# Kernel optimization log

Measured on AMD Instinct MI355X. Metric: run time of the kernel, lower is better.

Reference implementation:

```python
import jax, jax.numpy as jnp
import numpy as np

NEG_BIG = -9e15  # matches torch -9000000000000000.0

def setup_inputs() -> dict:
    key = jax.random.key(0)
    k1, k2, k3, k4 = jax.random.split(key, 4)
    B, N, F_IN, F_OUT = 8, 2048, 128, 64
    x = jax.random.normal(k1, (B, N, F_IN), dtype=jnp.float32)
    adj = jax.random.randint(k2, (B, N, N), 0, 2, dtype=jnp.int32)
    # xavier_uniform-style init for params
    limW = float(np.sqrt(6.0 / (F_IN + F_OUT)))
    W = jax.random.uniform(k3, (F_IN, F_OUT), minval=-limW, maxval=limW, dtype=jnp.float32)
    lima = float(np.sqrt(6.0 / (2 * F_OUT + 1)))
    a = jax.random.uniform(k4, (2 * F_OUT, 1), minval=-lima, maxval=lima, dtype=jnp.float32)
    return {"x": x, "adj": adj, "W": W, "a": a}

def reference(x, adj, W, a):
    # x: [B, N, F_in], adj: [B, N, N], W: [F_in, F_out], a: [2*F_out, 1]
    h = jnp.einsum('bnf,fo->bno', x, W)            # [B, N, F_out]
    F_out = W.shape[1]
    # The repeat/cat construction computes a_input[b,i,j] = [h_i ; h_j], so
    # a_input @ a decomposes into f1_i + f2_j without the O(N^2 * 2F) tensor.
    f1 = h @ a[:F_out, 0]                          # [B, N]
    f2 = h @ a[F_out:, 0]                          # [B, N]
    e = jnp.tanh(f1[:, :, None] + f2[:, None, :])  # [B, N, N]
    att = jnp.where(adj > 0, e, NEG_BIG)
    att = jax.nn.softmax(att, axis=2)              # [B, N, N]
    h_prime = jnp.einsum('bmn,bno->bmo', att, h)   # [B, N, F_out]
    return jax.nn.elu(h_prime)                     # concat=True branch
```

## Files before the change

### kernel.cpp

```cpp
#include <hip/hip_runtime.h>
#include <math.h>

#define BB 8
#define NN 2048
#define FIN 128
#define FOUT 64
#define TI 16
#define TJ 512
#define TJP (TJ + 8)
#define NTILE (NN / TJ)
#define NW (NN / 32)

typedef short bf16x8 __attribute__((ext_vector_type(8)));
typedef float f32x4 __attribute__((ext_vector_type(4)));

__device__ __forceinline__ float exp_tanh(float z) {
    float zc = fminf(fmaxf(z, -15.f), 15.f);
    float u = __expf(zc + zc);
    float tn = (u - 1.f) * __builtin_amdgcn_rcpf(u + 1.f);
    return __expf(tn);
}

__device__ __forceinline__ unsigned short f2bf(float x) {
    union { float f; unsigned u; } v; v.f = x;
    unsigned r = v.u + 0x7FFF + ((v.u >> 16) & 1);
    return (unsigned short)(r >> 16);
}

__global__ __launch_bounds__(256, 2) void gat_k1(const float* __restrict__ x,
                                                 const float* __restrict__ W,
                                                 const float* __restrict__ a,
                                                 unsigned short* __restrict__ ht,
                                                 float* __restrict__ f1,
                                                 float* __restrict__ f2) {
    __shared__ __attribute__((aligned(16))) float Wl[FIN][FOUT];
    __shared__ __attribute__((aligned(16))) float xs[16][FIN];
    int t = threadIdx.x;

    const float4* W4 = (const float4*)W;
    float4* Wl4 = (float4*)&Wl[0][0];
#pragma unroll
    for (int kk = 0; kk < 8; ++kk) Wl4[t + 256 * kk] = W4[t + 256 * kk];

    size_t row0 = (size_t)blockIdx.x * 16;
    const float4* x4 = (const float4*)(x + row0 * FIN);
    float4* xs4 = (float4*)&xs[0][0];
#pragma unroll
    for (int kk = 0; kk < 2; ++kk) xs4[t + 256 * kk] = x4[t + 256 * kk];
    __syncthreads();

    int c = t & 63;
    int rq = t >> 6;
    float acc[4] = {0.f, 0.f, 0.f, 0.f};
#pragma unroll 8
    for (int k = 0; k < FIN; ++k) {
        float wv = Wl[k][c];
        acc[0] = fmaf(xs[rq][k], wv, acc[0]);
        acc[1] = fmaf(xs[rq + 4][k], wv, acc[1]);
        acc[2] = fmaf(xs[rq + 8][k], wv, acc[2]);
        acc[3] = fmaf(xs[rq + 12][k], wv, acc[3]);
    }
    float a1c = a[c], a2c = a[FOUT + c];
#pragma unroll
    for (int m = 0; m < 4; ++m) {
        size_t bn = row0 + rq + 4 * m;
        int b = (int)(bn >> 11);
        int n = (int)(bn & 2047);
        ht[((size_t)b * FOUT + c) * NN + n] = f2bf(acc[m]);
        float p1 = acc[m] * a1c;
        float p2 = acc[m] * a2c;
#pragma unroll
        for (int off = 32; off > 0; off >>= 1) {
            p1 += __shfl_down(p1, off, 64);
            p2 += __shfl_down(p2, off, 64);
        }
        if (c == 0) { f1[bn] = p1; f2[bn] = p2; }
    }
}

__global__ __launch_bounds__(256) void gat_pack(const int* __restrict__ adj,
                                                unsigned int* __restrict__ adjm) {
    __shared__ __attribute__((aligned(4))) unsigned char nib[2048];
    int t = threadIdx.x;
    const int4* a4 = (const int4*)adj + (size_t)blockIdx.x * 2048;
#pragma unroll
    for (int kk = 0; kk < 8; ++kk) {
        int4 v = a4[t + 256 * kk];
        unsigned n = (unsigned)(v.x > 0) | ((unsigned)(v.y > 0) << 1) |
                     ((unsigned)(v.z > 0) << 2) | ((unsigned)(v.w > 0) << 3);
        nib[t + 256 * kk] = (unsigned char)n;
    }
    __syncthreads();
    const unsigned* nu = (const unsigned*)nib;
    unsigned u0 = nu[2 * t], u1 = nu[2 * t + 1];
    unsigned m = (u0 & 0xFu) | (((u0 >> 8) & 0xFu) << 4) |
                 (((u0 >> 16) & 0xFu) << 8) | (((u0 >> 24) & 0xFu) << 12) |
                 ((u1 & 0xFu) << 16) | (((u1 >> 8) & 0xFu) << 20) |
                 (((u1 >> 16) & 0xFu) << 24) | (((u1 >> 24) & 0xFu) << 28);
    adjm[(size_t)blockIdx.x * 256 + t] = m;
}

__global__ __launch_bounds__(256) void gat_k2(const unsigned int* __restrict__ adjm,
                                              const unsigned short* __restrict__ ht,
                                              const float* __restrict__ f1,
                                              const float* __restrict__ f2,
                                              float* __restrict__ accg,
                                              float* __restrict__ rs) {
    __shared__ __attribute__((aligned(16))) unsigned short pb[TI][TJP];
    __shared__ __attribute__((aligned(16))) float f2s[TJ];
    __shared__ float f1s[TI];
    __shared__ __attribute__((aligned(16))) unsigned int adjms[TI][16];

    int t = threadIdx.x;
    int i0 = blockIdx.x * TI;
    int j0 = blockIdx.y * TJ;
    int b = blockIdx.z;

    int lane = t & 63;
    int w = t >> 6;
    int mrow = lane & 15;
    int quad = lane >> 4;

    int j4 = t & 127;
    int r0 = t >> 7;

    int arow = t >> 4, awrd = t & 15;
    adjms[arow][awrd] =
        adjm[((size_t)b * NN + i0 + arow) * NW + (j0 >> 5) + awrd];

    ((float2*)f2s)[t] = ((const float2*)(f2 + (size_t)b * NN + j0))[t];
    if (t < TI) f1s[t] = f1[(size_t)b * NN + i0 + t];
    __syncthreads();

    float f1r[8];
    unsigned mrg[8];
#pragma unroll
    for (int kk = 0; kk < 8; ++kk) {
        f1r[kk] = f1s[r0 + 2 * kk];
        mrg[kk] = adjms[r0 + 2 * kk][j4 >> 3] >> ((j4 & 7) * 4);
    }

    float4 fv = ((const float4*)f2s)[j4];
    float ps[8];
#pragma unroll
    for (int kk = 0; kk < 8; ++kk) {
        unsigned mk = mrg[kk];
        float f1i = f1r[kk];
        float4 p;
        p.x = (mk & 1u) ? exp_tanh(f1i + fv.x) : 0.f;
        p.y = (mk & 2u) ? exp_tanh(f1i + fv.y) : 0.f;
        p.z = (mk & 4u) ? exp_tanh(f1i + fv.z) : 0.f;
        p.w = (mk & 8u) ? exp_tanh(f1i + fv.w) : 0.f;
        ps[kk] = p.x + p.y + p.z + p.w;
        ushort4 pk;
        pk.x = f2bf(p.x); pk.y = f2bf(p.y);
        pk.z = f2bf(p.z); pk.w = f2bf(p.w);
        *(ushort4*)&pb[r0 + 2 * kk][4 * j4] = pk;
    }
    __syncthreads();

    const unsigned short* hp =
        ht + ((size_t)b * FOUT + w * 16 + mrow) * NN + j0 + 8 * quad;
    const unsigned short* prow = &pb[mrow][8 * quad];
    f32x4 acc = {0.f, 0.f, 0.f, 0.f};
#pragma unroll 4
    for (int ch = 0; ch < TJ / 32; ++ch) {
        bf16x8 af = *(const bf16x8*)(prow + 32 * ch);
        bf16x8 bf = *(const bf16x8*)(hp + 32 * ch);
        acc = __builtin_amdgcn_mfma_f32_16x16x32_bf16(af, bf, acc, 0, 0, 0);
    }

#pragma unroll
    for (int kk = 0; kk < 8; ++kk) {
        float s = ps[kk];
#pragma unroll
        for (int off = 32; off > 0; off >>= 1) s += __shfl_down(s, off, 64);
        if (lane == 0)
            atomicAdd(&rs[(size_t)b * NN + i0 + r0 + 2 * kk], s);
    }
    float* ap = accg + ((size_t)b * NN + i0) * FOUT + w * 16 + mrow;
#pragma unroll
    for (int u = 0; u < 4; ++u) {
        int row = quad * 4 + u;
        atomicAdd(&ap[(size_t)row * FOUT], acc[u]);
    }
}

__global__ __launch_bounds__(256) void gat_k3(const float* __restrict__ accg,
                                              const float* __restrict__ rs,
                                              float* __restrict__ out) {
    int g4 = blockIdx.x * 256 + threadIdx.x;
    int row = g4 >> 4;
    float rinv = __builtin_amdgcn_rcpf(rs[row]);
    float4 v = ((const float4*)accg)[g4];
    float4 o;
    float sx = v.x * rinv; o.x = (sx > 0.f) ? sx : expm1f(sx);
    float sy = v.y * rinv; o.y = (sy > 0.f) ? sy : expm1f(sy);
    float sz = v.z * rinv; o.z = (sz > 0.f) ? sz : expm1f(sz);
    float sw = v.w * rinv; o.w = (sw > 0.f) ? sw : expm1f(sw);
    ((float4*)out)[g4] = o;
}

extern "C" void kernel_launch(void* const* d_in, const int* in_sizes, int n_in,
                              void* d_out, int out_size, void* d_ws, size_t ws_size,
                              hipStream_t stream) {
    const float* x   = (const float*)d_in[0];
    const int*   adj = (const int*)d_in[1];
    const float* W   = (const float*)d_in[2];
    const float* a   = (const float*)d_in[3];
    float* out = (float*)d_out;

    unsigned short* ht = (unsigned short*)d_ws;
    float* f1   = (float*)(ht + (size_t)BB * FOUT * NN);
    float* f2   = f1 + (size_t)BB * NN;
    float* accg = f2 + (size_t)BB * NN;
    float* rs   = accg + (size_t)BB * NN * FOUT;
    size_t used = (size_t)BB * FOUT * NN * 2
                + (size_t)BB * NN * 4 * 2
                + (size_t)BB * NN * FOUT * 4
                + (size_t)BB * NN * 4;
    size_t adjm_bytes = (size_t)BB * NN * (NN / 32) * 4;
    unsigned int* adjm = (ws_size >= used + adjm_bytes)
                             ? (unsigned int*)(rs + (size_t)BB * NN)
                             : (unsigned int*)d_out;
    hipMemsetAsync(accg, 0, ((size_t)BB * NN * FOUT + (size_t)BB * NN) * 4, stream);

    gat_pack<<<dim3((unsigned)((size_t)BB * NN * NN / 8192)), dim3(256), 0, stream>>>(adj, adjm);
    gat_k1<<<dim3(BB * NN / 16), dim3(256), 0, stream>>>(x, W, a, ht, f1, f2);
    gat_k2<<<dim3(NN / TI, NTILE, BB), dim3(256), 0, stream>>>(adjm, ht, f1, f2, accg, rs);
    gat_k3<<<dim3(BB * NN * FOUT / 1024), dim3(256), 0, stream>>>(accg, rs, out);
}
```

Baseline: 259.6 us.

## Fuse adjacency packing, attention aggregation and ELU into one kernel

```diff
diff --git a/kernel.cpp b/kernel.cpp
--- a/kernel.cpp
+++ b/kernel.cpp
@@ -9,7 +9,6 @@
 #define TJ 512
 #define TJP (TJ + 8)
 #define NTILE (NN / TJ)
-#define NW (NN / 32)
 
 typedef short bf16x8 __attribute__((ext_vector_type(8)));
 typedef float f32x4 __attribute__((ext_vector_type(4)));
@@ -78,43 +77,19 @@
     }
 }
 
-__global__ __launch_bounds__(256) void gat_pack(const int* __restrict__ adj,
-                                                unsigned int* __restrict__ adjm) {
-    __shared__ __attribute__((aligned(4))) unsigned char nib[2048];
-    int t = threadIdx.x;
-    const int4* a4 = (const int4*)adj + (size_t)blockIdx.x * 2048;
-#pragma unroll
-    for (int kk = 0; kk < 8; ++kk) {
-        int4 v = a4[t + 256 * kk];
-        unsigned n = (unsigned)(v.x > 0) | ((unsigned)(v.y > 0) << 1) |
-                     ((unsigned)(v.z > 0) << 2) | ((unsigned)(v.w > 0) << 3);
-        nib[t + 256 * kk] = (unsigned char)n;
-    }
-    __syncthreads();
-    const unsigned* nu = (const unsigned*)nib;
-    unsigned u0 = nu[2 * t], u1 = nu[2 * t + 1];
-    unsigned m = (u0 & 0xFu) | (((u0 >> 8) & 0xFu) << 4) |
-                 (((u0 >> 16) & 0xFu) << 8) | (((u0 >> 24) & 0xFu) << 12) |
-                 ((u1 & 0xFu) << 16) | (((u1 >> 8) & 0xFu) << 20) |
-                 (((u1 >> 16) & 0xFu) << 24) | (((u1 >> 24) & 0xFu) << 28);
-    adjm[(size_t)blockIdx.x * 256 + t] = m;
-}
-
-__global__ __launch_bounds__(256) void gat_k2(const unsigned int* __restrict__ adjm,
-                                              const unsigned short* __restrict__ ht,
-                                              const float* __restrict__ f1,
-                                              const float* __restrict__ f2,
-                                              float* __restrict__ accg,
-                                              float* __restrict__ rs) {
+__global__ __launch_bounds__(256) void gat_k2f(const int* __restrict__ adj,
+                                               const unsigned short* __restrict__ ht,
+                                               const float* __restrict__ f1,
+                                               const float* __restrict__ f2,
+                                               float* __restrict__ out) {
     __shared__ __attribute__((aligned(16))) unsigned short pb[TI][TJP];
     __shared__ __attribute__((aligned(16))) float f2s[TJ];
     __shared__ float f1s[TI];
-    __shared__ __attribute__((aligned(16))) unsigned int adjms[TI][16];
+    __shared__ float rsw[2][TI];
 
     int t = threadIdx.x;
     int i0 = blockIdx.x * TI;
-    int j0 = blockIdx.y * TJ;
-    int b = blockIdx.z;
+    int b = blockIdx.y;
 
     int lane = t & 63;
     int w = t >> 6;
@@ -124,50 +99,57 @@
     int j4 = t & 127;
     int r0 = t >> 7;
 
-    int arow = t >> 4, awrd = t & 15;
-    adjms[arow][awrd] =
-        adjm[((size_t)b * NN + i0 + arow) * NW + (j0 >> 5) + awrd];
-
-    ((float2*)f2s)[t] = ((const float2*)(f2 + (size_t)b * NN + j0))[t];
     if (t < TI) f1s[t] = f1[(size_t)b * NN + i0 + t];
     __syncthreads();
 
     float f1r[8];
-    unsigned mrg[8];
+    float ps[8];
 #pragma unroll
     for (int kk = 0; kk < 8; ++kk) {
         f1r[kk] = f1s[r0 + 2 * kk];
-        mrg[kk] = adjms[r0 + 2 * kk][j4 >> 3] >> ((j4 & 7) * 4);
+        ps[kk] = 0.f;
     }
+    f32x4 acc = {0.f, 0.f, 0.f, 0.f};
 
-    float4 fv = ((const float4*)f2s)[j4];
-    float ps[8];
+    for (int jt = 0; jt < NTILE; ++jt) {
+        int j0 = jt * TJ;
+
+        const int* adjbase = adj + (((size_t)b * NN + i0) * NN) + j0 + 4 * j4;
+        int4 avreg[8];
 #pragma unroll
-    for (int kk = 0; kk < 8; ++kk) {
-        unsigned mk = mrg[kk];
-        float f1i = f1r[kk];
-        float4 p;
-        p.x = (mk & 1u) ? exp_tanh(f1i + fv.x) : 0.f;
-        p.y = (mk & 2u) ? exp_tanh(f1i + fv.y) : 0.f;
-        p.z = (mk & 4u) ? exp_tanh(f1i + fv.z) : 0.f;
-        p.w = (mk & 8u) ? exp_tanh(f1i + fv.w) : 0.f;
-        ps[kk] = p.x + p.y + p.z + p.w;
-        ushort4 pk;
-        pk.x = f2bf(p.x); pk.y = f2bf(p.y);
-        pk.z = f2bf(p.z); pk.w = f2bf(p.w);
-        *(ushort4*)&pb[r0 + 2 * kk][4 * j4] = pk;
-    }
-    __syncthreads();
+        for (int kk = 0; kk < 8; ++kk)
+            avreg[kk] = *(const int4*)(adjbase + (size_t)(r0 + 2 * kk) * NN);
 
-    const unsigned short* hp =
-        ht + ((size_t)b * FOUT + w * 16 + mrow) * NN + j0 + 8 * quad;
-    const unsigned short* prow = &pb[mrow][8 * quad];
-    f32x4 acc = {0.f, 0.f, 0.f, 0.f};
+        ((float2*)f2s)[t] = ((const float2*)(f2 + (size_t)b * NN + j0))[t];
+        __syncthreads();
+
+        float4 fv = ((const float4*)f2s)[j4];
+#pragma unroll
+        for (int kk = 0; kk < 8; ++kk) {
+            int4 av = avreg[kk];
+            float f1i = f1r[kk];
+            float4 p;
+            p.x = (av.x > 0) ? exp_tanh(f1i + fv.x) : 0.f;
+            p.y = (av.y > 0) ? exp_tanh(f1i + fv.y) : 0.f;
+            p.z = (av.z > 0) ? exp_tanh(f1i + fv.z) : 0.f;
+            p.w = (av.w > 0) ? exp_tanh(f1i + fv.w) : 0.f;
+            ps[kk] += p.x + p.y + p.z + p.w;
+            ushort4 pk;
+            pk.x = f2bf(p.x); pk.y = f2bf(p.y);
+            pk.z = f2bf(p.z); pk.w = f2bf(p.w);
+            *(ushort4*)&pb[r0 + 2 * kk][4 * j4] = pk;
+        }
+        __syncthreads();
+
+        const unsigned short* hp =
+            ht + ((size_t)b * FOUT + w * 16 + mrow) * NN + j0 + 8 * quad;
+        const unsigned short* prow = &pb[mrow][8 * quad];
 #pragma unroll 4
-    for (int ch = 0; ch < TJ / 32; ++ch) {
-        bf16x8 af = *(const bf16x8*)(prow + 32 * ch);
-        bf16x8 bf = *(const bf16x8*)(hp + 32 * ch);
-        acc = __builtin_amdgcn_mfma_f32_16x16x32_bf16(af, bf, acc, 0, 0, 0);
+        for (int ch = 0; ch < TJ / 32; ++ch) {
+            bf16x8 af = *(const bf16x8*)(prow + 32 * ch);
+            bf16x8 bf = *(const bf16x8*)(hp + 32 * ch);
+            acc = __builtin_amdgcn_mfma_f32_16x16x32_bf16(af, bf, acc, 0, 0, 0);
+        }
     }
 
 #pragma unroll
@@ -175,30 +157,18 @@
         float s = ps[kk];
 #pragma unroll
         for (int off = 32; off > 0; off >>= 1) s += __shfl_down(s, off, 64);
-        if (lane == 0)
-            atomicAdd(&rs[(size_t)b * NN + i0 + r0 + 2 * kk], s);
+        if (lane == 0) rsw[w & 1][r0 + 2 * kk] = s;
     }
-    float* ap = accg + ((size_t)b * NN + i0) * FOUT + w * 16 + mrow;
+    __syncthreads();
+
+    float* op = out + ((size_t)b * NN + i0) * FOUT + w * 16 + mrow;
 #pragma unroll
     for (int u = 0; u < 4; ++u) {
         int row = quad * 4 + u;
-        atomicAdd(&ap[(size_t)row * FOUT], acc[u]);
+        float rinv = __builtin_amdgcn_rcpf(rsw[0][row] + rsw[1][row]);
+        float sx = acc[u] * rinv;
+        op[(size_t)row * FOUT] = (sx > 0.f) ? sx : expm1f(sx);
     }
-}
-
-__global__ __launch_bounds__(256) void gat_k3(const float* __restrict__ accg,
-                                              const float* __restrict__ rs,
-                                              float* __restrict__ out) {
-    int g4 = blockIdx.x * 256 + threadIdx.x;
-    int row = g4 >> 4;
-    float rinv = __builtin_amdgcn_rcpf(rs[row]);
-    float4 v = ((const float4*)accg)[g4];
-    float4 o;
-    float sx = v.x * rinv; o.x = (sx > 0.f) ? sx : expm1f(sx);
-    float sy = v.y * rinv; o.y = (sy > 0.f) ? sy : expm1f(sy);
-    float sz = v.z * rinv; o.z = (sz > 0.f) ? sz : expm1f(sz);
-    float sw = v.w * rinv; o.w = (sw > 0.f) ? sw : expm1f(sw);
-    ((float4*)out)[g4] = o;
 }
 
 extern "C" void kernel_launch(void* const* d_in, const int* in_sizes, int n_in,
@@ -213,20 +183,7 @@
     unsigned short* ht = (unsigned short*)d_ws;
     float* f1   = (float*)(ht + (size_t)BB * FOUT * NN);
     float* f2   = f1 + (size_t)BB * NN;
-    float* accg = f2 + (size_t)BB * NN;
-    float* rs   = accg + (size_t)BB * NN * FOUT;
-    size_t used = (size_t)BB * FOUT * NN * 2
-                + (size_t)BB * NN * 4 * 2
-                + (size_t)BB * NN * FOUT * 4
-                + (size_t)BB * NN * 4;
-    size_t adjm_bytes = (size_t)BB * NN * (NN / 32) * 4;
-    unsigned int* adjm = (ws_size >= used + adjm_bytes)
-                             ? (unsigned int*)(rs + (size_t)BB * NN)
-                             : (unsigned int*)d_out;
-    hipMemsetAsync(accg, 0, ((size_t)BB * NN * FOUT + (size_t)BB * NN) * 4, stream);
 
-    gat_pack<<<dim3((unsigned)((size_t)BB * NN * NN / 8192)), dim3(256), 0, stream>>>(adj, adjm);
     gat_k1<<<dim3(BB * NN / 16), dim3(256), 0, stream>>>(x, W, a, ht, f1, f2);
-    gat_k2<<<dim3(NN / TI, NTILE, BB), dim3(256), 0, stream>>>(adjm, ht, f1, f2, accg, rs);
-    gat_k3<<<dim3(BB * NN * FOUT / 1024), dim3(256), 0, stream>>>(accg, rs, out);
+    gat_k2f<<<dim3(NN / TI, BB), dim3(256), 0, stream>>>(adj, ht, f1, f2, out);
 }
```

Result: faster. 227.7 us (-12.3%).
